# Kernel tuning notes

Measured on AMD Instinct MI355X. Metric: run time of the kernel, lower is better.

Reference implementation:

```python
import jax, jax.numpy as jnp
import numpy as np

N, C, H, W = 8, 32, 48, 48
S, K, OC = 2, 3, 32  # scale_int, kernel_size, out_channels
HID = 256
FEAT = C * K * K  # 288


def setup_inputs() -> dict:
    key = jax.random.key(0)
    ks = jax.random.split(key, 5)
    F_LR = jax.random.normal(ks[0], (N, C, H, W), dtype=jnp.float32)
    v = jax.random.normal(ks[1], (H * S * W * S, 3), dtype=jnp.float32)
    w1 = jax.random.normal(ks[2], (3, HID), dtype=jnp.float32) * 0.2
    b1 = jnp.zeros((HID,), dtype=jnp.float32)
    w2 = jax.random.normal(ks[3], (HID, FEAT * OC), dtype=jnp.float32) * 0.02
    b2 = jnp.zeros((FEAT * OC,), dtype=jnp.float32)
    return {"F_LR": F_LR, "v": v, "w1": w1, "b1": b1, "w2": w2, "b2": b2}


def _unfold(x, k):
    # torch F.unfold(x, k, padding=1): (N, C*k*k, H*W), channel-major then (ki,kj)
    n, c, h, w = x.shape
    xp = jnp.pad(x, ((0, 0), (0, 0), (1, 1), (1, 1)))
    cols = [xp[:, :, i:i + h, j:j + w] for i in range(k) for j in range(k)]
    p = jnp.stack(cols, axis=2)  # (N, C, k*k, H, W)
    return p.reshape(n, c * k * k, h * w)


def reference(F_LR, v, w1, b1, w2, b2):
    n = F_LR.shape[0]
    # weight prediction MLP
    hmid = jax.nn.relu(v @ w1 + b1)
    W_pred = hmid @ w2 + b2  # (H*S*W*S, C*K*K*OC)
    # reshape like torch: view(H,S,W,S,FEAT,OC).permute(1,3,0,2,4,5) -> (S*S, H*W, FEAT, OC)
    Wt = (W_pred.reshape(H, S, W, S, FEAT, OC)
          .transpose(1, 3, 0, 2, 4, 5)
          .reshape(S * S, H * W, FEAT, OC))
    # add_dimensions replicates F_LR S*S times, so patches are shared across p
    pat = _unfold(F_LR, K)  # (N, FEAT, H*W)
    # per-pixel tiny matmul: out[n,p,l,o] = sum_f pat[n,f,l] * Wt[p,l,f,o]
    out = jnp.einsum('nfl,plfo->nplo', pat, Wt)  # (N, S*S, H*W, OC)
    # assemble upsampled image: p=(sh,sw), pixel (h*S+sh, w*S+sw)
    out = (out.reshape(n, S, S, H, W, OC)
           .transpose(0, 5, 3, 1, 4, 2)
           .reshape(n, OC, S * H, S * W))
    # integer scale => create_mask is all-True, masked_select is identity
    return out
```

## Files before the change

### kernel.cpp

```cpp
#include <hip/hip_runtime.h>
#include <hip/hip_bf16.h>

#define NN    8
#define CC    32
#define HH    48
#define WW    48
#define OCC   32
#define HID   256
#define FEAT  288
#define RTOT  9216
#define COLS  9216
#define XUP   96
#define YUP   96
#define OUTSZ (NN*OCC*XUP*YUP)

using bf16x8 = __attribute__((ext_vector_type(8))) __bf16;
using bf16x4 = __attribute__((ext_vector_type(4))) __bf16;
using f32x4  = __attribute__((ext_vector_type(4))) float;

__global__ void prep_hmid(const float* __restrict__ v, const float* __restrict__ w1,
                          const float* __restrict__ b1, __hip_bfloat16* __restrict__ hmidp) {
  int r = blockIdx.x;
  int t = threadIdx.x;
  float v0 = v[r*3+0], v1 = v[r*3+1], v2 = v[r*3+2];
  float val = v0*w1[t] + v1*w1[HID+t] + v2*w1[2*HID+t] + b1[t];
  val = fmaxf(val, 0.0f);
  int dst = ((r>>4)*8 + (t>>5))*512 + ((t>>3)&3)*128 + (r&15)*8 + (t&7);
  hmidp[dst] = __float2bfloat16(val);
}

__global__ void prep_w2(const float* __restrict__ w2, __hip_bfloat16* __restrict__ w2p) {
  int idx = blockIdx.x*256 + threadIdx.x;
  int k   = idx / COLS;
  int col = idx % COLS;
  float val = w2[idx];
  int colchunk = col >> 7;
  int cg   = (col >> 4) & 7;
  int lane = (((k>>3)&3)<<4) | (col & 15);
  int kb   = k >> 5;
  int i    = k & 7;
  int dst  = (((colchunk*8 + kb)*8 + cg)*64 + lane)*8 + i;
  w2p[dst] = __float2bfloat16(val);
}

#define BARRIER_LGKM() do {                              \
    asm volatile("s_waitcnt lgkmcnt(0)" ::: "memory");   \
    __builtin_amdgcn_sched_barrier(0);                   \
    __builtin_amdgcn_s_barrier();                        \
  } while (0)

#define ISSUE_HALF(SET, CH, H) do {                                              \
    const char* _b = w2base + ((size_t)((CH)*8 + (H)*4))*8192 + wv*2048          \
                     + (size_t)lane*16;                                          \
    _Pragma("unroll")                                                            \
    for (int _i = 0; _i < 4; ++_i) {                                             \
      SET[0][_i] = *(const bf16x8*)(_b + _i*8192);                               \
      SET[1][_i] = *(const bf16x8*)(_b + _i*8192 + 1024);                        \
    }                                                                            \
  } while (0)

__launch_bounds__(256, 2)
__global__ void fused_main(const float* __restrict__ F_LR,
                           const __hip_bfloat16* __restrict__ hmidp,
                           const __hip_bfloat16* __restrict__ w2p,
                           const float* __restrict__ b2,
                           float* __restrict__ outp,
                           int G, int nch) {
  extern __shared__ __align__(16) char smem[];
  __bf16* patB  = (__bf16*)smem;
  float*  wc    = (float*)(smem + 27648);
  __bf16* biasL = (__bf16*)(smem + 44032);

  const int tid  = threadIdx.x;
  const int lane = tid & 63;
  const int wv   = tid >> 6;
  const int blk  = blockIdx.x;
  int rowtile, g;
  if (G == 2) {
    int xcd = blk & 7;
    int j   = blk >> 3;
    g       = xcd & 1;
    rowtile = (xcd >> 1)*72 + j;
  } else {
    rowtile = blk;
    g       = 0;
  }
  const int X  = rowtile / 3;
  const int Yh = rowtile - X*3;
  const int h  = X >> 1;
  const int w0 = Yh * 16;
  const int l15 = lane & 15;
  const int qt  = lane >> 4;
  const int oc  = lane & 31;
  const int nh  = lane >> 5;

  const char* w2base = (const char*)w2p + (size_t)g*nch*65536;

  bf16x8 a[2][8];
  {
    const bf16x8* ap = reinterpret_cast<const bf16x8*>(hmidp) + (size_t)rowtile*1024 + lane;
    #pragma unroll
    for (int mg = 0; mg < 2; ++mg)
      #pragma unroll
      for (int kb = 0; kb < 8; ++kb) a[mg][kb] = ap[(mg*8 + kb)*64];
  }

  for (int i = tid; i < nch*128; i += 256)
    biasL[i] = (__bf16)b2[g*nch*128 + i];

  {
    const int n = tid >> 5, c = tid & 31;
    const float* fsrc = F_LR + ((size_t)(n*CC + c)*HH)*WW;
    #pragma unroll
    for (int ki = 0; ki < 3; ++ki) {
      int hh = h - 1 + ki;
      bool hok = (unsigned)hh < (unsigned)HH;
      #pragma unroll
      for (int wi = 0; wi < 18; ++wi) {
        int ww = w0 - 1 + wi;
        float val = (hok && (unsigned)ww < (unsigned)WW) ? fsrc[hh*WW + ww] : 0.f;
        patB[((c*3 + ki)*18 + wi)*8 + n] = (__bf16)val;
      }
    }
  }
  BARRIER_LGKM();

  float oacc[8][4];
  #pragma unroll
  for (int i = 0; i < 8; ++i)
    { oacc[i][0]=0.f; oacc[i][1]=0.f; oacc[i][2]=0.f; oacc[i][3]=0.f; }

  bf16x8 bA[2][4], bB[2][4];
  ISSUE_HALF(bA, 0, 0);
  ISSUE_HALF(bB, 0, 1);

  for (int ch = 0; ch < nch; ++ch) {
    f32x4 acc00 = {0,0,0,0}, acc01 = {0,0,0,0}, acc10 = {0,0,0,0}, acc11 = {0,0,0,0};

    #pragma unroll
    for (int s = 0; s < 4; ++s) {
      acc00 = __builtin_amdgcn_mfma_f32_16x16x32_bf16(a[0][s], bA[0][s], acc00, 0,0,0);
      acc01 = __builtin_amdgcn_mfma_f32_16x16x32_bf16(a[0][s], bA[1][s], acc01, 0,0,0);
      acc10 = __builtin_amdgcn_mfma_f32_16x16x32_bf16(a[1][s], bA[0][s], acc10, 0,0,0);
      acc11 = __builtin_amdgcn_mfma_f32_16x16x32_bf16(a[1][s], bA[1][s], acc11, 0,0,0);
    }
    if (ch + 1 < nch) { ISSUE_HALF(bA, ch+1, 0); }

    #pragma unroll
    for (int s = 0; s < 4; ++s) {
      acc00 = __builtin_amdgcn_mfma_f32_16x16x32_bf16(a[0][4+s], bB[0][s], acc00, 0,0,0);
      acc01 = __builtin_amdgcn_mfma_f32_16x16x32_bf16(a[0][4+s], bB[1][s], acc01, 0,0,0);
      acc10 = __builtin_amdgcn_mfma_f32_16x16x32_bf16(a[1][4+s], bB[0][s], acc10, 0,0,0);
      acc11 = __builtin_amdgcn_mfma_f32_16x16x32_bf16(a[1][4+s], bB[1][s], acc11, 0,0,0);
    }
    if (ch + 1 < nch) { ISSUE_HALF(bB, ch+1, 1); }

    {
      float bias0 = (float)biasL[ch*128 + wv*32 + l15];
      float bias1 = (float)biasL[ch*128 + wv*32 + 16 + l15];
      #pragma unroll
      for (int mg = 0; mg < 2; ++mg) {
        #pragma unroll
        for (int ng = 0; ng < 2; ++ng) {
          f32x4 A = (mg==0) ? (ng==0?acc00:acc01) : (ng==0?acc10:acc11);
          float bb = ng ? bias1 : bias0;
          A[0]+=bb; A[1]+=bb; A[2]+=bb; A[3]+=bb;
          int ocx  = ng*16 + l15;
          int ridx = (mg*16 + qt*4) ^ ((ocx&7)<<2);
          *(f32x4*)&wc[wv*1024 + ocx*32 + ridx] = A;
        }
      }
    }
    BARRIER_LGKM();

    const int swz = (oc & 7) << 2;
    #pragma unroll
    for (int fl = 0; fl < 4; ++fl) {
      const int f   = (g*nch + ch)*4 + fl;
      const int c   = f / 9;
      const int rem = f - c*9;
      const int ki  = rem / 3;
      const int kj  = rem - ki*3;
      const f32x4 wlo = *(const f32x4*)&wc[fl*1024 + oc*32 + ((wv*8    ) ^ swz)];
      const f32x4 whi = *(const f32x4*)&wc[fl*1024 + oc*32 + ((wv*8 + 4) ^ swz)];
      const __bf16* pbase = patB + (c*3 + ki)*18*8 + nh*4;
      #pragma unroll
      for (int rrh = 0; rrh < 4; ++rrh) {
        bf16x4 pq = *(const bf16x4*)(pbase + (wv*4 + rrh + kj)*8);
        float w0v = (rrh < 2) ? ((rrh == 0) ? wlo[0] : wlo[2]) : ((rrh == 2) ? whi[0] : whi[2]);
        float w1v = (rrh < 2) ? ((rrh == 0) ? wlo[1] : wlo[3]) : ((rrh == 2) ? whi[1] : whi[3]);
        #pragma unroll
        for (int q = 0; q < 4; ++q) {
          float pv = (float)pq[q];
          oacc[rrh*2][q]   += w0v * pv;
          oacc[rrh*2+1][q] += w1v * pv;
        }
      }
    }
    BARRIER_LGKM();
  }

  float* OP = outp + (size_t)g*OUTSZ;
  #pragma unroll
  for (int q = 0; q < 4; ++q) {
    int n = nh*4 + q;
    f32x4 v0, v1;
    v0[0]=oacc[0][q]; v0[1]=oacc[1][q]; v0[2]=oacc[2][q]; v0[3]=oacc[3][q];
    v1[0]=oacc[4][q]; v1[1]=oacc[5][q]; v1[2]=oacc[6][q]; v1[3]=oacc[7][q];
    float* dst = OP + (((size_t)(n*OCC + oc)*XUP + X)*YUP + Yh*32 + wv*8);
    *(f32x4*)dst     = v0;
    *(f32x4*)(dst+4) = v1;
  }
}

__global__ void reduce2(const float* __restrict__ P, float* __restrict__ out) {
  int i = blockIdx.x*256 + threadIdx.x;
  if (i < OUTSZ/4) {
    f32x4 a = ((const f32x4*)P)[i];
    f32x4 b = ((const f32x4*)(P + OUTSZ))[i];
    ((f32x4*)out)[i] = a + b;
  }
}

extern "C" void kernel_launch(void* const* d_in, const int* in_sizes, int n_in,
                              void* d_out, int out_size, void* d_ws, size_t ws_size,
                              hipStream_t stream) {
  const float* F_LR = (const float*)d_in[0];
  const float* v    = (const float*)d_in[1];
  const float* w1   = (const float*)d_in[2];
  const float* b1   = (const float*)d_in[3];
  const float* w2   = (const float*)d_in[4];
  const float* b2   = (const float*)d_in[5];
  float* out = (float*)d_out;

  const size_t prepBytes = (size_t)RTOT*HID*2;
  const size_t need2 = 2*prepBytes + 2ull*OUTSZ*4;
  const int G   = (ws_size >= need2) ? 2 : 1;
  const int nch = 72 / G;

  __hip_bfloat16* hmidp = (__hip_bfloat16*)d_ws;
  __hip_bfloat16* w2p   = (__hip_bfloat16*)((char*)d_ws + prepBytes);
  float* P = (float*)((char*)d_ws + 2*prepBytes);
  float* target = (G == 2) ? P : out;

  const size_t shmem = 27648 + 16384 + (size_t)nch*128*2;

  hipLaunchKernelGGL(prep_hmid, dim3(RTOT), dim3(HID), 0, stream, v, w1, b1, hmidp);
  hipLaunchKernelGGL(prep_w2,   dim3((HID*COLS)/256), dim3(256), 0, stream, w2, w2p);
  hipLaunchKernelGGL(fused_main, dim3(288*G), dim3(256), shmem, stream,
                     F_LR, hmidp, w2p, b2, target, G, nch);
  if (G == 2)
    hipLaunchKernelGGL(reduce2, dim3(OUTSZ/4/256), dim3(256), 0, stream, P, out);
}
```

Measured before the change: 176.1 us.

## Split feature reduction four ways, use packed FMA accumulators, raise occupancy

The fused kernel now splits the 72-chunk feature reduction into four groups instead of two, launching four times the row-tile grid and summing four partial outputs in a generalized reduce kernel. The occupancy hint goes from 2 to 3 blocks per CU, and the per-pixel accumulation is rewritten with float2 vectors so the compiler can emit packed FMAs. More blocks should fill the GPU better than 576. The cost is more partial-output traffic and a heavier final reduction, plus register pressure that could cause spills under the tighter launch bound.

```diff
diff --git a/kernel.cpp b/kernel.cpp
--- a/kernel.cpp
+++ b/kernel.cpp
@@ -17,6 +17,7 @@
 using bf16x8 = __attribute__((ext_vector_type(8))) __bf16;
 using bf16x4 = __attribute__((ext_vector_type(4))) __bf16;
 using f32x4  = __attribute__((ext_vector_type(4))) float;
+using f32x2  = __attribute__((ext_vector_type(2))) float;
 
 __global__ void prep_hmid(const float* __restrict__ v, const float* __restrict__ w1,
                           const float* __restrict__ b1, __hip_bfloat16* __restrict__ hmidp) {
@@ -59,7 +60,7 @@
     }                                                                            \
   } while (0)
 
-__launch_bounds__(256, 2)
+__launch_bounds__(256, 3)
 __global__ void fused_main(const float* __restrict__ F_LR,
                            const __hip_bfloat16* __restrict__ hmidp,
                            const __hip_bfloat16* __restrict__ w2p,
@@ -76,7 +77,12 @@
   const int wv   = tid >> 6;
   const int blk  = blockIdx.x;
   int rowtile, g;
-  if (G == 2) {
+  if (G == 4) {
+    int xcd = blk & 7;
+    int j   = blk >> 3;
+    g       = xcd & 3;
+    rowtile = (xcd >> 2)*144 + j;
+  } else if (G == 2) {
     int xcd = blk & 7;
     int j   = blk >> 3;
     g       = xcd & 1;
@@ -125,10 +131,9 @@
   }
   BARRIER_LGKM();
 
-  float oacc[8][4];
+  f32x2 oacc2[8][2];
   #pragma unroll
-  for (int i = 0; i < 8; ++i)
-    { oacc[i][0]=0.f; oacc[i][1]=0.f; oacc[i][2]=0.f; oacc[i][3]=0.f; }
+  for (int i = 0; i < 8; ++i) { oacc2[i][0] = 0.f; oacc2[i][1] = 0.f; }
 
   bf16x8 bA[2][4], bB[2][4];
   ISSUE_HALF(bA, 0, 0);
@@ -183,18 +188,18 @@
       const int kj  = rem - ki*3;
       const f32x4 wlo = *(const f32x4*)&wc[fl*1024 + oc*32 + ((wv*8    ) ^ swz)];
       const f32x4 whi = *(const f32x4*)&wc[fl*1024 + oc*32 + ((wv*8 + 4) ^ swz)];
-      const __bf16* pbase = patB + (c*3 + ki)*18*8 + nh*4;
+      const __bf16* pbase = patB + (c*3 + ki)*144 + nh*4;
       #pragma unroll
       for (int rrh = 0; rrh < 4; ++rrh) {
         bf16x4 pq = *(const bf16x4*)(pbase + (wv*4 + rrh + kj)*8);
+        f32x2 p01; p01[0] = (float)pq[0]; p01[1] = (float)pq[1];
+        f32x2 p23; p23[0] = (float)pq[2]; p23[1] = (float)pq[3];
         float w0v = (rrh < 2) ? ((rrh == 0) ? wlo[0] : wlo[2]) : ((rrh == 2) ? whi[0] : whi[2]);
         float w1v = (rrh < 2) ? ((rrh == 0) ? wlo[1] : wlo[3]) : ((rrh == 2) ? whi[1] : whi[3]);
-        #pragma unroll
-        for (int q = 0; q < 4; ++q) {
-          float pv = (float)pq[q];
-          oacc[rrh*2][q]   += w0v * pv;
-          oacc[rrh*2+1][q] += w1v * pv;
-        }
+        oacc2[rrh*2][0]   += p01 * w0v;
+        oacc2[rrh*2][1]   += p23 * w0v;
+        oacc2[rrh*2+1][0] += p01 * w1v;
+        oacc2[rrh*2+1][1] += p23 * w1v;
       }
     }
     BARRIER_LGKM();
@@ -205,20 +210,23 @@
   for (int q = 0; q < 4; ++q) {
     int n = nh*4 + q;
     f32x4 v0, v1;
-    v0[0]=oacc[0][q]; v0[1]=oacc[1][q]; v0[2]=oacc[2][q]; v0[3]=oacc[3][q];
-    v1[0]=oacc[4][q]; v1[1]=oacc[5][q]; v1[2]=oacc[6][q]; v1[3]=oacc[7][q];
+    v0[0]=oacc2[0][q>>1][q&1]; v0[1]=oacc2[1][q>>1][q&1];
+    v0[2]=oacc2[2][q>>1][q&1]; v0[3]=oacc2[3][q>>1][q&1];
+    v1[0]=oacc2[4][q>>1][q&1]; v1[1]=oacc2[5][q>>1][q&1];
+    v1[2]=oacc2[6][q>>1][q&1]; v1[3]=oacc2[7][q>>1][q&1];
     float* dst = OP + (((size_t)(n*OCC + oc)*XUP + X)*YUP + Yh*32 + wv*8);
     *(f32x4*)dst     = v0;
     *(f32x4*)(dst+4) = v1;
   }
 }
 
-__global__ void reduce2(const float* __restrict__ P, float* __restrict__ out) {
+__global__ void reduceG(const float* __restrict__ P, float* __restrict__ out, int G) {
   int i = blockIdx.x*256 + threadIdx.x;
   if (i < OUTSZ/4) {
-    f32x4 a = ((const f32x4*)P)[i];
-    f32x4 b = ((const f32x4*)(P + OUTSZ))[i];
-    ((f32x4*)out)[i] = a + b;
+    f32x4 s = ((const f32x4*)P)[i];
+    for (int p = 1; p < G; ++p)
+      s += ((const f32x4*)(P + (size_t)p*OUTSZ))[i];
+    ((f32x4*)out)[i] = s;
   }
 }
 
@@ -234,14 +242,15 @@
   float* out = (float*)d_out;
 
   const size_t prepBytes = (size_t)RTOT*HID*2;
+  const size_t need4 = 2*prepBytes + 4ull*OUTSZ*4;
   const size_t need2 = 2*prepBytes + 2ull*OUTSZ*4;
-  const int G   = (ws_size >= need2) ? 2 : 1;
+  const int G   = (ws_size >= need4) ? 4 : (ws_size >= need2) ? 2 : 1;
   const int nch = 72 / G;
 
   __hip_bfloat16* hmidp = (__hip_bfloat16*)d_ws;
   __hip_bfloat16* w2p   = (__hip_bfloat16*)((char*)d_ws + prepBytes);
   float* P = (float*)((char*)d_ws + 2*prepBytes);
-  float* target = (G == 2) ? P : out;
+  float* target = (G > 1) ? P : out;
 
   const size_t shmem = 27648 + 16384 + (size_t)nch*128*2;
 
@@ -249,6 +258,6 @@
   hipLaunchKernelGGL(prep_w2,   dim3((HID*COLS)/256), dim3(256), 0, stream, w2, w2p);
   hipLaunchKernelGGL(fused_main, dim3(288*G), dim3(256), shmem, stream,
                      F_LR, hmidp, w2p, b2, target, G, nch);
-  if (G == 2)
-    hipLaunchKernelGGL(reduce2, dim3(OUTSZ/4/256), dim3(256), 0, stream, P, out);
-}
+  if (G > 1)
+    hipLaunchKernelGGL(reduceG, dim3(OUTSZ/4/256), dim3(256), 0, stream, P, out, G);
+}
```

New measurement: 287.3 us. 1.63x slower.
